# Kernel tuning notes

Measured on AMD Instinct MI355X. Metric: run time of the kernel, lower is better.

Reference implementation:

```python
import jax, jax.numpy as jnp
import numpy as np

# multi-scale pyramid (low2high: lowest resolution first), d_model etc. from module defaults
SHAPES = ((8, 8), (16, 16), (32, 32), (64, 64))
D, HEADS, DH, PTS, NLV, NLAYERS, DFF = 256, 8, 32, 4, 4, 6, 1024
L_TOTAL = sum(h * w for h, w in SHAPES)  # 5440
B = 4


def _ref_points():
    # normalized (x, y) pixel centers per level, concatenated -> [L_TOTAL, 2]
    pts = []
    for (H, W) in SHAPES:
        ry = (jnp.arange(H, dtype=jnp.float32) + 0.5) / H
        rx = (jnp.arange(W, dtype=jnp.float32) + 0.5) / W
        gy, gx = jnp.meshgrid(ry, rx, indexing='ij')
        pts.append(jnp.stack([gx.ravel(), gy.ravel()], -1))
    return jnp.concatenate(pts, 0)


def _lev_ids():
    return jnp.concatenate([jnp.full((h * w,), l, dtype=jnp.int32)
                            for l, (h, w) in enumerate(SHAPES)])


def _layer_norm(x, g, b):
    m = jnp.mean(x, -1, keepdims=True)
    v = jnp.mean((x - m) ** 2, -1, keepdims=True)
    return g * (x - m) * jax.lax.rsqrt(v + 1e-5) + b


def _ms_deform_attn(q, src, ref, w_off, b_off, w_attn, b_attn, w_val, b_val, w_out, b_out):
    Bq, L, _ = q.shape
    v = (src @ w_val + b_val).reshape(Bq, L, HEADS, DH)
    off = (q @ w_off + b_off).reshape(Bq, L, HEADS, NLV, PTS, 2)
    aw = jax.nn.softmax((q @ w_attn + b_attn).reshape(Bq, L, HEADS, NLV * PTS), -1)
    aw = aw.reshape(Bq, L, HEADS, NLV, PTS)
    # offset normalizer is (W, H) per level
    norm = jnp.array([[w, h] for (h, w) in SHAPES], dtype=q.dtype)
    loc = ref[None, :, None, None, None, :] + off / norm[None, None, None, :, None, :]
    out = jnp.zeros((Bq, L, HEADS, DH), q.dtype)
    start = 0
    for l, (H_, W_) in enumerate(SHAPES):
        vl = v[:, start:start + H_ * W_].transpose(0, 2, 1, 3)  # [B, heads, HW, dh]
        # grid_sample(align_corners=False): pixel coord = loc * size - 0.5
        x = loc[:, :, :, l, :, 0] * W_ - 0.5  # [B, L, heads, P]
        y = loc[:, :, :, l, :, 1] * H_ - 0.5
        x0 = jnp.floor(x).astype(jnp.int32)
        y0 = jnp.floor(y).astype(jnp.int32)
        fx = x - x0
        fy = y - y0

        def corner(ix, iy, w):
            inb = ((ix >= 0) & (ix < W_) & (iy >= 0) & (iy < H_)).astype(q.dtype)
            idx = jnp.clip(iy, 0, H_ - 1) * W_ + jnp.clip(ix, 0, W_ - 1)
            idx = idx.transpose(0, 2, 1, 3).reshape(Bq, HEADS, L * PTS, 1)
            g = jnp.take_along_axis(vl, idx, axis=2)  # [B, heads, L*P, dh]
            wt = (w * inb).transpose(0, 2, 1, 3).reshape(Bq, HEADS, L * PTS, 1)
            return g * wt

        samp = (corner(x0, y0, (1 - fx) * (1 - fy))
                + corner(x0 + 1, y0, fx * (1 - fy))
                + corner(x0, y0 + 1, (1 - fx) * fy)
                + corner(x0 + 1, y0 + 1, fx * fy))
        samp = samp.reshape(Bq, HEADS, L, PTS, DH)
        out = out + jnp.einsum('blhp,bhlpd->blhd', aw[:, :, :, l, :], samp)
        start += H_ * W_
    return out.reshape(Bq, L, D) @ w_out + b_out


def setup_inputs() -> dict:
    key = jax.random.key(0)
    ks = jax.random.split(key, 16)
    s = 0.02
    inp = {
        'src': jax.random.normal(ks[0], (B, L_TOTAL, D), jnp.float32),
        'pos': jax.random.normal(ks[1], (B, L_TOTAL, D), jnp.float32),
        'level_embed': jax.random.normal(ks[2], (NLV, D), jnp.float32),
        'w_off': jax.random.normal(ks[3], (NLAYERS, D, HEADS * NLV * PTS * 2), jnp.float32) * s,
        'b_off': jnp.zeros((NLAYERS, HEADS * NLV * PTS * 2), jnp.float32),
        'w_attn': jax.random.normal(ks[4], (NLAYERS, D, HEADS * NLV * PTS), jnp.float32) * s,
        'b_attn': jnp.zeros((NLAYERS, HEADS * NLV * PTS), jnp.float32),
        'w_val': jax.random.normal(ks[5], (NLAYERS, D, D), jnp.float32) * s,
        'b_val': jnp.zeros((NLAYERS, D), jnp.float32),
        'w_out': jax.random.normal(ks[6], (NLAYERS, D, D), jnp.float32) * s,
        'b_out': jnp.zeros((NLAYERS, D), jnp.float32),
        'ln1_g': jnp.ones((NLAYERS, D), jnp.float32),
        'ln1_b': jnp.zeros((NLAYERS, D), jnp.float32),
        'w_ff1': jax.random.normal(ks[7], (NLAYERS, D, DFF), jnp.float32) * s,
        'b_ff1': jnp.zeros((NLAYERS, DFF), jnp.float32),
        'w_ff2': jax.random.normal(ks[8], (NLAYERS, DFF, D), jnp.float32) * s,
        'b_ff2': jnp.zeros((NLAYERS, D), jnp.float32),
        'ln2_g': jnp.ones((NLAYERS, D), jnp.float32),
        'ln2_b': jnp.zeros((NLAYERS, D), jnp.float32),
    }
    return inp


def reference(src, pos, level_embed, w_off, b_off, w_attn, b_attn, w_val, b_val,
              w_out, b_out, ln1_g, ln1_b, w_ff1, b_ff1, w_ff2, b_ff2, ln2_g, ln2_b):
    # lvl_pos_embed = pos + level_embed[level-of-token] (masks all False -> valid_ratios == 1)
    lvl_pos = pos + level_embed[_lev_ids()]
    ref = _ref_points().astype(src.dtype)
    x = src
    for i in range(NLAYERS):
        q = x + lvl_pos
        x2 = _ms_deform_attn(q, x, ref, w_off[i], b_off[i], w_attn[i], b_attn[i],
                             w_val[i], b_val[i], w_out[i], b_out[i])
        x = _layer_norm(x + x2, ln1_g[i], ln1_b[i])
        ff = jax.nn.relu(x @ w_ff1[i] + b_ff1[i]) @ w_ff2[i] + b_ff2[i]
        x = _layer_norm(x + ff, ln2_g[i], ln2_b[i])
    return x
```

## Files before the change

### kernel.cpp

```cpp
#include <hip/hip_runtime.h>

#define LTOT 5440
#define NTOK 21760

typedef float  f32x4  __attribute__((ext_vector_type(4)));
typedef short  short8 __attribute__((ext_vector_type(8)));

__device__ __forceinline__ unsigned short f2bf(float f) {
  unsigned int u = __float_as_uint(f);
  u += 0x7FFF + ((u >> 16) & 1);
  return (unsigned short)(u >> 16);
}
__device__ __forceinline__ float bf2f(unsigned short u) {
  return __uint_as_float(((unsigned int)u) << 16);
}

__global__ void wconv(const float* __restrict__ w_off, const float* __restrict__ w_attn,
                      const float* __restrict__ w_val, const float* __restrict__ w_out,
                      const float* __restrict__ w_ff1, const float* __restrict__ w_ff2,
                      unsigned short* __restrict__ dst) {
  int tid = blockIdx.x * 256 + threadIdx.x;
  const int PER = 753664;
  if (tid >= 6 * PER) return;
  int layer = tid / PER;
  int rem = tid - layer * PER;
  int base, K, N;
  const float* src;
  if (rem < 65536)       { base = 0;      K = 256;  N = 256;  src = w_off; }
  else if (rem < 98304)  { base = 65536;  K = 256;  N = 128;  src = w_attn; }
  else if (rem < 163840) { base = 98304;  K = 256;  N = 256;  src = w_val; }
  else if (rem < 229376) { base = 163840; K = 256;  N = 256;  src = w_out; }
  else if (rem < 491520) { base = 229376; K = 256;  N = 1024; src = w_ff1; }
  else                   { base = 491520; K = 1024; N = 256;  src = w_ff2; }
  int local = rem - base;
  int n = local / K, k = local - n * K;
  dst[tid] = f2bf(src[(size_t)layer * K * N + (size_t)k * N + n]);
}

__global__ void bpack(const float* __restrict__ b_off, const float* __restrict__ b_attn,
                      float* __restrict__ fb) {
  int l = blockIdx.x, t = threadIdx.x;
  fb[l * 384 + t] = (t < 256) ? b_off[l * 256 + t] : b_attn[l * 128 + t - 256];
}

__global__ void prep(const float* __restrict__ src, const float* __restrict__ pos,
                     const float* __restrict__ lev_emb, float* __restrict__ x,
                     unsigned short* __restrict__ xb, unsigned short* __restrict__ qb) {
  int i = blockIdx.x * 256 + threadIdx.x;
  int d4 = i & 63;
  int tok = (i >> 6) % LTOT;
  int lev = (tok < 64) ? 0 : (tok < 320) ? 1 : (tok < 1344) ? 2 : 3;
  float4 s = ((const float4*)src)[i];
  float4 pv = ((const float4*)pos)[i];
  float4 lv = ((const float4*)lev_emb)[lev * 64 + d4];
  ((float4*)x)[i] = s;
  ushort4 o;
  o.x = f2bf(s.x); o.y = f2bf(s.y); o.z = f2bf(s.z); o.w = f2bf(s.w);
  ((ushort4*)xb)[i] = o;
  ushort4 q;
  q.x = f2bf(s.x + pv.x + lv.x);
  q.y = f2bf(s.y + pv.y + lv.y);
  q.z = f2bf(s.z + pv.z + lv.z);
  q.w = f2bf(s.w + pv.w + lv.w);
  ((ushort4*)qb)[i] = q;
}

template<bool RELU, bool OBF16>
__global__ __launch_bounds__(256) void gemm_tn(
    const unsigned short* __restrict__ A, const unsigned short* __restrict__ Wt,
    const float* __restrict__ bias, void* __restrict__ Cout,
    int M, int N, int K) {
  __shared__ __align__(16) unsigned short a_lds[128 * 64];
  __shared__ __align__(16) unsigned short b_lds[128 * 64];
  int m0 = blockIdx.x * 128;
  int n0 = blockIdx.y * 128;
  int t = threadIdx.x;
  int w = t >> 6, l = t & 63;
  int wr = (w >> 1) * 64, wc = (w & 1) * 64;
  int lr = l & 15, lk = (l >> 4) * 8;

  f32x4 acc[4][4] = {};

  for (int k0 = 0; k0 < K; k0 += 64) {
#pragma unroll
    for (int i = 0; i < 4; ++i) {
      int c = i * 256 + t;
      int row = c >> 3, off8 = (c & 7) * 8;
      const unsigned short* gp = A + (size_t)(m0 + row) * K + k0 + off8;
      __builtin_amdgcn_global_load_lds(
          (const __attribute__((address_space(1))) void*)gp,
          (__attribute__((address_space(3))) void*)(a_lds + c * 8), 16, 0, 0);
    }
#pragma unroll
    for (int i = 0; i < 4; ++i) {
      int c = i * 256 + t;
      int row = c >> 3, off8 = (c & 7) * 8;
      const unsigned short* gp = Wt + (size_t)(n0 + row) * K + k0 + off8;
      __builtin_amdgcn_global_load_lds(
          (const __attribute__((address_space(1))) void*)gp,
          (__attribute__((address_space(3))) void*)(b_lds + c * 8), 16, 0, 0);
    }
    __syncthreads();
#pragma unroll
    for (int kk = 0; kk < 64; kk += 32) {
      short8 af[4], bfr[4];
#pragma unroll
      for (int m = 0; m < 4; ++m)
        af[m] = *(const short8*)(a_lds + (wr + m * 16 + lr) * 64 + kk + lk);
#pragma unroll
      for (int n = 0; n < 4; ++n)
        bfr[n] = *(const short8*)(b_lds + (wc + n * 16 + lr) * 64 + kk + lk);
#pragma unroll
      for (int m = 0; m < 4; ++m)
#pragma unroll
        for (int n = 0; n < 4; ++n)
          acc[m][n] = __builtin_amdgcn_mfma_f32_16x16x32_bf16(af[m], bfr[n], acc[m][n], 0, 0, 0);
    }
    __syncthreads();
  }

  int rb = (l >> 4) * 4;
#pragma unroll
  for (int n = 0; n < 4; ++n) {
    int col = n0 + wc + n * 16 + lr;
    float bv = bias[col];
#pragma unroll
    for (int m = 0; m < 4; ++m) {
#pragma unroll
      for (int r = 0; r < 4; ++r) {
        int row = m0 + wr + m * 16 + rb + r;
        float v = acc[m][n][r] + bv;
        if (RELU) v = fmaxf(v, 0.0f);
        if (OBF16) ((unsigned short*)Cout)[(size_t)row * N + col] = f2bf(v);
        else       ((float*)Cout)[(size_t)row * N + col] = v;
      }
    }
  }
}

__global__ __launch_bounds__(256) void ms_sample(
    const float* __restrict__ offattn, const unsigned short* __restrict__ vb,
    unsigned short* __restrict__ samp) {
  __shared__ int   sIdx[128 * 4];
  __shared__ float sWt[128 * 4];
  int bid = blockIdx.x;
  int bl = (bid & 7) * (NTOK / 8) + (bid >> 3);
  int t = threadIdx.x;
  int l = bl % LTOT;
  int bbase = (bl - l) * 256;
  if (t < 128) {
    float logit = offattn[(size_t)bl * 384 + 256 + t];
    float mx = logit;
#pragma unroll
    for (int o = 1; o < 16; o <<= 1) mx = fmaxf(mx, __shfl_xor(mx, o));
    float e = __expf(logit - mx);
    float ssum = e;
#pragma unroll
    for (int o = 1; o < 16; o <<= 1) ssum += __shfl_xor(ssum, o);
    float aw = e / ssum;

    int lev = (t >> 2) & 3;
    int lev_q = (l < 64) ? 0 : (l < 320) ? 1 : (l < 1344) ? 2 : 3;
    int start_q = (lev_q == 0) ? 0 : (lev_q == 1) ? 64 : (lev_q == 2) ? 320 : 1344;
    int shq = lev_q + 3;
    int r = l - start_q;
    int Wq = 1 << shq;
    int iy = r >> shq, ix = r & (Wq - 1);
    float invWq = 1.0f / (float)Wq;
    float refx = ((float)ix + 0.5f) * invWq;
    float refy = ((float)iy + 0.5f) * invWq;
    int iW = 8 << lev;
    float Wl = (float)iW;
    int start_l = (lev == 0) ? 0 : (lev == 1) ? 64 : (lev == 2) ? 320 : 1344;
    float ox = offattn[(size_t)bl * 384 + 2 * t];
    float oy = offattn[(size_t)bl * 384 + 2 * t + 1];
    float gx = refx * Wl + ox - 0.5f;
    float gy = refy * Wl + oy - 0.5f;
    float flx = floorf(gx), fly = floorf(gy);
    int x0 = (int)flx, y0 = (int)fly;
    float fx = gx - flx, fy = gy - fly;
#pragma unroll
    for (int c = 0; c < 4; ++c) {
      int cx = x0 + (c & 1);
      int cy = y0 + (c >> 1);
      int inb = (cx >= 0) && (cx < iW) && (cy >= 0) && (cy < iW);
      int cxc = cx < 0 ? 0 : (cx > iW - 1 ? iW - 1 : cx);
      int cyc = cy < 0 ? 0 : (cy > iW - 1 ? iW - 1 : cy);
      float wx = (c & 1) ? fx : 1.0f - fx;
      float wy = (c & 2) ? fy : 1.0f - fy;
      sIdx[t * 4 + c] = (start_l + cyc * iW + cxc) * 256;
      sWt[t * 4 + c] = inb ? aw * wx * wy : 0.0f;
    }
  }
  __syncthreads();
  int h = t >> 5;
  int sbase = h * 64;
  float acc0 = 0.0f, acc1 = 0.0f;
#pragma unroll
  for (int s = 0; s < 16; ++s) {
    float w0 = sWt[sbase + s * 4 + 0]; int i0 = sIdx[sbase + s * 4 + 0];
    float w1 = sWt[sbase + s * 4 + 1]; int i1 = sIdx[sbase + s * 4 + 1];
    float w2 = sWt[sbase + s * 4 + 2]; int i2 = sIdx[sbase + s * 4 + 2];
    float w3 = sWt[sbase + s * 4 + 3]; int i3 = sIdx[sbase + s * 4 + 3];
    acc0 = fmaf(w0, bf2f(vb[bbase + i0 + t]), acc0);
    acc1 = fmaf(w1, bf2f(vb[bbase + i1 + t]), acc1);
    acc0 = fmaf(w2, bf2f(vb[bbase + i2 + t]), acc0);
    acc1 = fmaf(w3, bf2f(vb[bbase + i3 + t]), acc1);
  }
  samp[(size_t)bl * 256 + t] = f2bf(acc0 + acc1);
}

template<bool QADD>
__global__ __launch_bounds__(256) void ln_fused(
    const float* __restrict__ xin, const float* __restrict__ yin,
    const float* __restrict__ g, const float* __restrict__ bb,
    const float* __restrict__ pos, const float* __restrict__ lev_emb,
    float* __restrict__ xout, unsigned short* __restrict__ xbout,
    unsigned short* __restrict__ qbout) {
  int row = blockIdx.x * 4 + (threadIdx.x >> 6);
  int lane = threadIdx.x & 63;
  size_t base = (size_t)row * 64 + lane;
  float4 xv = ((const float4*)xin)[base];
  float4 yv = ((const float4*)yin)[base];
  float4 tv;
  tv.x = xv.x + yv.x; tv.y = xv.y + yv.y; tv.z = xv.z + yv.z; tv.w = xv.w + yv.w;
  float s = tv.x + tv.y + tv.z + tv.w;
  float s2 = tv.x * tv.x + tv.y * tv.y + tv.z * tv.z + tv.w * tv.w;
#pragma unroll
  for (int o = 1; o < 64; o <<= 1) {
    s += __shfl_xor(s, o, 64);
    s2 += __shfl_xor(s2, o, 64);
  }
  float mean = s * (1.0f / 256.0f);
  float var = s2 * (1.0f / 256.0f) - mean * mean;
  float rstd = rsqrtf(var + 1e-5f);
  float4 gv = ((const float4*)g)[lane];
  float4 bv = ((const float4*)bb)[lane];
  float4 o;
  o.x = gv.x * (tv.x - mean) * rstd + bv.x;
  o.y = gv.y * (tv.y - mean) * rstd + bv.y;
  o.z = gv.z * (tv.z - mean) * rstd + bv.z;
  o.w = gv.w * (tv.w - mean) * rstd + bv.w;
  ((float4*)xout)[base] = o;
  ushort4 ob;
  ob.x = f2bf(o.x); ob.y = f2bf(o.y); ob.z = f2bf(o.z); ob.w = f2bf(o.w);
  ((ushort4*)xbout)[base] = ob;
  if (QADD) {
    int tok = row % LTOT;
    int lev = (tok < 64) ? 0 : (tok < 320) ? 1 : (tok < 1344) ? 2 : 3;
    float4 pv = ((const float4*)pos)[base];
    float4 lv = ((const float4*)lev_emb)[lev * 64 + lane];
    ushort4 q;
    q.x = f2bf(o.x + pv.x + lv.x);
    q.y = f2bf(o.y + pv.y + lv.y);
    q.z = f2bf(o.z + pv.z + lv.z);
    q.w = f2bf(o.w + pv.w + lv.w);
    ((ushort4*)qbout)[base] = q;
  }
}

extern "C" void kernel_launch(void* const* d_in, const int* in_sizes, int n_in,
                              void* d_out, int out_size, void* d_ws, size_t ws_size,
                              hipStream_t stream) {
  (void)in_sizes; (void)n_in; (void)out_size; (void)ws_size;
  const float* src     = (const float*)d_in[0];
  const float* pos     = (const float*)d_in[1];
  const float* lev_emb = (const float*)d_in[2];
  const float* w_off   = (const float*)d_in[3];
  const float* b_off   = (const float*)d_in[4];
  const float* w_attn  = (const float*)d_in[5];
  const float* b_attn  = (const float*)d_in[6];
  const float* w_val   = (const float*)d_in[7];
  const float* b_val   = (const float*)d_in[8];
  const float* w_out   = (const float*)d_in[9];
  const float* b_out   = (const float*)d_in[10];
  const float* ln1_g   = (const float*)d_in[11];
  const float* ln1_b   = (const float*)d_in[12];
  const float* w_ff1   = (const float*)d_in[13];
  const float* b_ff1   = (const float*)d_in[14];
  const float* w_ff2   = (const float*)d_in[15];
  const float* b_ff2   = (const float*)d_in[16];
  const float* ln2_g   = (const float*)d_in[17];
  const float* ln2_b   = (const float*)d_in[18];

  char* ws = (char*)d_ws;
  float*          x     = (float*)(ws + 0);
  float*          y     = (float*)(ws + 22282240);
  unsigned short* xb    = (unsigned short*)(ws + 44564480);
  unsigned short* qb    = (unsigned short*)(ws + 55705600);
  unsigned short* sampb = (unsigned short*)(ws + 55705600);
  float*          offat = (float*)(ws + 66846720);
  unsigned short* vb    = (unsigned short*)(ws + 100270080);
  unsigned short* h1    = (unsigned short*)(ws + 66846720);
  unsigned short* wT    = (unsigned short*)(ws + 111411200);
  float*          fb    = (float*)(ws + 120455168);

  wconv<<<17664, 256, 0, stream>>>(w_off, w_attn, w_val, w_out, w_ff1, w_ff2, wT);
  bpack<<<6, 384, 0, stream>>>(b_off, b_attn, fb);
  prep<<<5440, 256, 0, stream>>>(src, pos, lev_emb, x, xb, qb);

  for (int i = 0; i < 6; ++i) {
    const unsigned short* wl = wT + (size_t)i * 753664;
    gemm_tn<false, false><<<dim3(170, 3), 256, 0, stream>>>(qb, wl + 0,      fb + i * 384,     (void*)offat, NTOK, 384, 256);
    gemm_tn<false, true ><<<dim3(170, 2), 256, 0, stream>>>(xb, wl + 98304,  b_val + i * 256,  (void*)vb,    NTOK, 256, 256);
    ms_sample<<<NTOK, 256, 0, stream>>>(offat, vb, sampb);
    gemm_tn<false, false><<<dim3(170, 2), 256, 0, stream>>>(sampb, wl + 163840, b_out + i * 256, (void*)y,   NTOK, 256, 256);
    ln_fused<false><<<5440, 256, 0, stream>>>(x, y, ln1_g + i * 256, ln1_b + i * 256, pos, lev_emb, x, xb, qb);
    gemm_tn<true,  true ><<<dim3(170, 8), 256, 0, stream>>>(xb, wl + 229376, b_ff1 + i * 1024, (void*)h1,    NTOK, 1024, 256);
    gemm_tn<false, false><<<dim3(170, 2), 256, 0, stream>>>(h1, wl + 491520, b_ff2 + i * 256,  (void*)y,     NTOK, 256, 1024);
    float* xo = (i == 5) ? (float*)d_out : x;
    if (i < 5)
      ln_fused<true ><<<5440, 256, 0, stream>>>(x, y, ln2_g + i * 256, ln2_b + i * 256, pos, lev_emb, xo, xb, qb);
    else
      ln_fused<false><<<5440, 256, 0, stream>>>(x, y, ln2_g + i * 256, ln2_b + i * 256, pos, lev_emb, xo, xb, qb);
  }
}
```

Measured before the change: 1.288 ms.

## Restructure deformable sampling gather with vectorized 4-channel loads and split-K reduction

The sampling kernel now packs each weight and its byte offset into one shared-memory uint2. Each thread loads 4 bf16 channels at once (8 bytes) instead of a single 2-byte value. The 64 sample points of a head are split across 4 thread groups, with rotated access order to spread LDS bank use, and the partial sums are combined with cross-lane shuffles. This is meant to cut the number of gather instructions and widen memory transactions, at the cost of shuffle reductions and only a quarter of lanes doing the store.

```diff
diff --git a/kernel.cpp b/kernel.cpp
--- a/kernel.cpp
+++ b/kernel.cpp
@@ -4,6 +4,7 @@
 #define NTOK 21760
 
 typedef float  f32x4  __attribute__((ext_vector_type(4)));
+typedef float  f32x2  __attribute__((ext_vector_type(2)));
 typedef short  short8 __attribute__((ext_vector_type(8)));
 
 __device__ __forceinline__ unsigned short f2bf(float f) {
@@ -141,8 +142,7 @@
 __global__ __launch_bounds__(256) void ms_sample(
     const float* __restrict__ offattn, const unsigned short* __restrict__ vb,
     unsigned short* __restrict__ samp) {
-  __shared__ int   sIdx[128 * 4];
-  __shared__ float sWt[128 * 4];
+  __shared__ __align__(16) uint2 sWI[512];
   int bid = blockIdx.x;
   int bl = (bid & 7) * (NTOK / 8) + (bid >> 3);
   int t = threadIdx.x;
@@ -188,26 +188,49 @@
       int cyc = cy < 0 ? 0 : (cy > iW - 1 ? iW - 1 : cy);
       float wx = (c & 1) ? fx : 1.0f - fx;
       float wy = (c & 2) ? fy : 1.0f - fy;
-      sIdx[t * 4 + c] = (start_l + cyc * iW + cxc) * 256;
-      sWt[t * 4 + c] = inb ? aw * wx * wy : 0.0f;
+      float wgt = inb ? aw * wx * wy : 0.0f;
+      unsigned int idxb = (unsigned int)(start_l + cyc * iW + cxc) * 512u;
+      sWI[t * 4 + c] = make_uint2(__float_as_uint(wgt), idxb);
     }
   }
   __syncthreads();
-  int h = t >> 5;
-  int sbase = h * 64;
-  float acc0 = 0.0f, acc1 = 0.0f;
-#pragma unroll
-  for (int s = 0; s < 16; ++s) {
-    float w0 = sWt[sbase + s * 4 + 0]; int i0 = sIdx[sbase + s * 4 + 0];
-    float w1 = sWt[sbase + s * 4 + 1]; int i1 = sIdx[sbase + s * 4 + 1];
-    float w2 = sWt[sbase + s * 4 + 2]; int i2 = sIdx[sbase + s * 4 + 2];
-    float w3 = sWt[sbase + s * 4 + 3]; int i3 = sIdx[sbase + s * 4 + 3];
-    acc0 = fmaf(w0, bf2f(vb[bbase + i0 + t]), acc0);
-    acc1 = fmaf(w1, bf2f(vb[bbase + i1 + t]), acc1);
-    acc0 = fmaf(w2, bf2f(vb[bbase + i2 + t]), acc0);
-    acc1 = fmaf(w3, bf2f(vb[bbase + i3 + t]), acc1);
-  }
-  samp[(size_t)bl * 256 + t] = f2bf(acc0 + acc1);
+  int h = t >> 5, j = t & 31;
+  int q = j >> 3, p = j & 7;
+  int rotp = ((h & 1) << 2) | q;
+  const uint2* wiBase = sWI + h * 64 + q * 16;
+  unsigned int chb = (unsigned int)(h * 32 + p * 4) * 2u;
+  const char* vB = (const char*)(vb + bbase);
+  f32x2 a01 = {0.0f, 0.0f}, a23 = {0.0f, 0.0f};
+#pragma unroll
+  for (int kp = 0; kp < 8; ++kp) {
+    int kq = ((kp + rotp) & 7) * 2;
+    uint4 wi2 = *(const uint4*)(wiBase + kq);
+    float w0 = __uint_as_float(wi2.x);
+    float w1 = __uint_as_float(wi2.z);
+    uint2 u0 = *(const uint2*)(vB + (wi2.y + chb));
+    uint2 u1 = *(const uint2*)(vB + (wi2.w + chb));
+    f32x2 v01a = { __uint_as_float(u0.x << 16), __uint_as_float(u0.x & 0xffff0000u) };
+    f32x2 v23a = { __uint_as_float(u0.y << 16), __uint_as_float(u0.y & 0xffff0000u) };
+    f32x2 w0v = {w0, w0};
+    a01 = __builtin_elementwise_fma(w0v, v01a, a01);
+    a23 = __builtin_elementwise_fma(w0v, v23a, a23);
+    f32x2 v01b = { __uint_as_float(u1.x << 16), __uint_as_float(u1.x & 0xffff0000u) };
+    f32x2 v23b = { __uint_as_float(u1.y << 16), __uint_as_float(u1.y & 0xffff0000u) };
+    f32x2 w1v = {w1, w1};
+    a01 = __builtin_elementwise_fma(w1v, v01b, a01);
+    a23 = __builtin_elementwise_fma(w1v, v23b, a23);
+  }
+  float c0 = a01.x, c1 = a01.y, c2 = a23.x, c3 = a23.y;
+  c0 += __shfl_xor(c0, 8);  c1 += __shfl_xor(c1, 8);
+  c2 += __shfl_xor(c2, 8);  c3 += __shfl_xor(c3, 8);
+  c0 += __shfl_xor(c0, 16); c1 += __shfl_xor(c1, 16);
+  c2 += __shfl_xor(c2, 16); c3 += __shfl_xor(c3, 16);
+  if (q == 0) {
+    uint2 pk;
+    pk.x = (unsigned int)f2bf(c0) | ((unsigned int)f2bf(c1) << 16);
+    pk.y = (unsigned int)f2bf(c2) | ((unsigned int)f2bf(c3) << 16);
+    *(uint2*)(samp + (size_t)bl * 256 + h * 32 + p * 4) = pk;
+  }
 }
 
 template<bool QADD>
```

New measurement: 1.205 ms. -6.5%, faster.
